# Kernel tuning notes

Hardware: AMD Instinct MI355X
Metric: run time of the kernel (lower is better)

## Reference

```python
import jax, jax.numpy as jnp
import numpy as np

HIDDEN = 50
INPUT = 4

def setup_inputs() -> dict:
    key = jax.random.key(0)
    ks = jax.random.split(key, 7)
    B, T = 4096, 512
    s_ih = 1.0 / np.sqrt(HIDDEN)
    return {
        "x": jax.random.normal(ks[0], (B, T, INPUT), dtype=jnp.float32),
        "W_ih": jax.random.uniform(ks[1], (4 * HIDDEN, INPUT), jnp.float32, -s_ih, s_ih),
        "W_hh": jax.random.uniform(ks[2], (4 * HIDDEN, HIDDEN), jnp.float32, -s_ih, s_ih),
        "b_ih": jax.random.uniform(ks[3], (4 * HIDDEN,), jnp.float32, -s_ih, s_ih),
        "b_hh": jax.random.uniform(ks[4], (4 * HIDDEN,), jnp.float32, -s_ih, s_ih),
        "W_fc": jax.random.uniform(ks[5], (1, HIDDEN), jnp.float32, -s_ih, s_ih),
        "b_fc": jax.random.uniform(ks[6], (1,), jnp.float32, -s_ih, s_ih),
    }

def reference(x, W_ih, W_hh, b_ih, b_hh, W_fc, b_fc):
    B = x.shape[0]
    b = b_ih + b_hh  # fold biases once
    # precompute input projection for all timesteps: [B,T,4H]
    x_proj = jnp.einsum('btd,gd->btg', x, W_ih) + b
    h0 = jnp.zeros((B, HIDDEN), x.dtype)
    c0 = jnp.zeros((B, HIDDEN), x.dtype)

    def step(carry, xp_t):
        h, c = carry
        gates = xp_t + h @ W_hh.T  # [B,4H]
        i, f, g, o = jnp.split(gates, 4, axis=-1)  # PyTorch gate order i,f,g,o
        i = jax.nn.sigmoid(i)
        f = jax.nn.sigmoid(f)
        g = jnp.tanh(g)
        o = jax.nn.sigmoid(o)
        c_new = f * c + i * g
        h_new = o * jnp.tanh(c_new)
        return (h_new, c_new), None

    (h_T, _), _ = jax.lax.scan(step, (h0, c0), jnp.swapaxes(x_proj, 0, 1))
    # fc applied to last timestep only (out[:, -1, :])
    return h_T @ W_fc.T + b_fc  # [B,1]
```

## Files before the change

### kernel.cpp

```cpp
#include <hip/hip_runtime.h>


#define HID  50
#define NROW 200
#define TT   512
#define NIN  4
#define BT   16
#define KD   72
#define XSTR 17
#define NW   8

typedef float f32x4 __attribute__((ext_vector_type(4)));
typedef short s16x8 __attribute__((ext_vector_type(8)));

__device__ __forceinline__ unsigned short f2bf(float f) {
    unsigned u = __builtin_bit_cast(unsigned, f);
    return (unsigned short)((u + 0x7FFF + ((u >> 16) & 1)) >> 16);
}
__device__ __forceinline__ float fast_sigmoid(float v) {
    float e = __builtin_amdgcn_exp2f(v * -1.442695040888963f);
    return __builtin_amdgcn_rcpf(1.0f + e);
}
__device__ __forceinline__ float fast_tanh(float v) {
    float e = __builtin_amdgcn_exp2f(v * -2.885390081777927f);
    return 2.0f * __builtin_amdgcn_rcpf(1.0f + e) - 1.0f;
}

__device__ __forceinline__ float wval(const float* W_hh, const float* W_ih,
                                      int rowp, int kp) {
    if (rowp >= NROW) return 0.0f;
    const int u = rowp >> 2, g = rowp & 3;
    if (kp < HID)              return W_hh[(g * HID + u) * HID + kp];
    if (kp >= 56 && kp < 60)   return W_ih[(g * HID + u) * NIN + (kp - 56)];
    return 0.0f;
}

__global__ __launch_bounds__(64 * NW, 2)
void lstm_mfma4(const float* __restrict__ x,
                const float* __restrict__ W_ih,
                const float* __restrict__ W_hh,
                const float* __restrict__ b_ih,
                const float* __restrict__ b_hh,
                const float* __restrict__ W_fc,
                const float* __restrict__ b_fc,
                float* __restrict__ out)
{
    __shared__ __align__(16) unsigned short buf[2][BT][KD];
    __shared__ uint2 xpl[TT * XSTR];
    __shared__ float red[BT];

    const int tid = threadIdx.x;
    const int w   = tid >> 6;
    const int l   = tid & 63;
    const int lr  = l & 15;
    const int lg  = l >> 4;
    const int b0  = blockIdx.x * BT;

    for (int i = tid; i < 2 * BT * KD; i += 64 * NW)
        ((unsigned short*)buf)[i] = 0;
    if (tid < BT) red[tid] = 0.0f;

    {
        const float4* xs = (const float4*)(x + (size_t)b0 * TT * NIN);
#pragma unroll
        for (int it = 0; it < (TT * BT) / (64 * NW); ++it) {
            const int e = tid + it * 64 * NW;
            const float4 v = xs[e];
            unsigned lo, hi;
            asm("v_cvt_pk_bf16_f32 %0, %1, %2" : "=v"(lo) : "v"(v.x), "v"(v.y));
            asm("v_cvt_pk_bf16_f32 %0, %1, %2" : "=v"(hi) : "v"(v.z), "v"(v.w));
            const int brel = e >> 9, t = e & (TT - 1);
            xpl[t * XSTR + brel] = make_uint2(lo, hi);
        }
    }

    const bool two = (w < 5);
    const int  T0  = two ? w : (w + 5);
    const int  T1  = w + 5;

    s16x8 af0[2], af1[2];
    f32x4 bias0, bias1 = {0.f, 0.f, 0.f, 0.f};
    float wfc0 = 0.0f, wfc1 = 0.0f;
    {
        const int rowp = 16 * T0 + lr;
#pragma unroll
        for (int kh = 0; kh < 2; ++kh) {
            s16x8 f;
#pragma unroll
            for (int j = 0; j < 8; ++j)
                f[j] = (short)f2bf(wval(W_hh, W_ih, rowp, 32 * kh + 8 * lg + j));
            af0[kh] = f;
        }
#pragma unroll
        for (int r = 0; r < 4; ++r) {
            const int rr = 16 * T0 + 4 * lg + r;
            bias0[r] = (rr < NROW) ? (b_ih[(rr & 3) * HID + (rr >> 2)] +
                                      b_hh[(rr & 3) * HID + (rr >> 2)]) : 0.0f;
        }
        const int u = 4 * T0 + lg;
        wfc0 = (u < HID) ? W_fc[u] : 0.0f;
    }
    if (two) {
        const int rowp = 16 * T1 + lr;
#pragma unroll
        for (int kh = 0; kh < 2; ++kh) {
            s16x8 f;
#pragma unroll
            for (int j = 0; j < 8; ++j)
                f[j] = (short)f2bf(wval(W_hh, W_ih, rowp, 32 * kh + 8 * lg + j));
            af1[kh] = f;
        }
#pragma unroll
        for (int r = 0; r < 4; ++r) {
            const int rr = 16 * T1 + 4 * lg + r;
            bias1[r] = (rr < NROW) ? (b_ih[(rr & 3) * HID + (rr >> 2)] +
                                      b_hh[(rr & 3) * HID + (rr >> 2)]) : 0.0f;
        }
        const int u = 4 * T1 + lg;
        wfc1 = (u < HID) ? W_fc[u] : 0.0f;
    }
    __syncthreads();

    float c0 = 0.f, h0 = 0.f, c1 = 0.f, h1 = 0.f;

    for (int t = 0; t < TT; ++t) {
        const int p = t & 1;

        const s16x8 bf0v = *(const s16x8*)&buf[p][lr][8 * lg];
        s16x8 bf1v;
        if (lg == 3) {
            const uint2 xv = xpl[t * XSTR + lr];
            const uint4 tmp = {xv.x, xv.y, 0u, 0u};
            bf1v = __builtin_bit_cast(s16x8, tmp);
        } else {
            bf1v = *(const s16x8*)&buf[p][lr][32 + 8 * lg];
        }

        f32x4 a0 = bias0;
        a0 = __builtin_amdgcn_mfma_f32_16x16x32_bf16(af0[0], bf0v, a0, 0, 0, 0);
        a0 = __builtin_amdgcn_mfma_f32_16x16x32_bf16(af0[1], bf1v, a0, 0, 0, 0);
        f32x4 a1;
        if (two) {
            a1 = bias1;
            a1 = __builtin_amdgcn_mfma_f32_16x16x32_bf16(af1[0], bf0v, a1, 0, 0, 0);
            a1 = __builtin_amdgcn_mfma_f32_16x16x32_bf16(af1[1], bf1v, a1, 0, 0, 0);
        }

        {
            const float gi = fast_sigmoid(a0[0]);
            const float gf = fast_sigmoid(a0[1]);
            const float gg = fast_tanh(a0[2]);
            const float go = fast_sigmoid(a0[3]);
            c0 = gf * c0 + gi * gg;
            h0 = go * fast_tanh(c0);
            buf[p ^ 1][lr][4 * T0 + lg] = f2bf(h0);
        }
        if (two) {
            const float gi = fast_sigmoid(a1[0]);
            const float gf = fast_sigmoid(a1[1]);
            const float gg = fast_tanh(a1[2]);
            const float go = fast_sigmoid(a1[3]);
            c1 = gf * c1 + gi * gg;
            h1 = go * fast_tanh(c1);
            buf[p ^ 1][lr][4 * T1 + lg] = f2bf(h1);
        }
        __syncthreads();
    }

    float partial = wfc0 * h0 + wfc1 * h1;
    partial += __shfl_down(partial, 32);
    partial += __shfl_down(partial, 16);
    if (l < 16) atomicAdd(&red[l], partial);
    __syncthreads();
    if (tid < BT) out[b0 + tid] = red[tid] + b_fc[0];
}

extern "C" void kernel_launch(void* const* d_in, const int* in_sizes, int n_in,
                              void* d_out, int out_size, void* d_ws, size_t ws_size,
                              hipStream_t stream) {
    const float* x    = (const float*)d_in[0];
    const float* W_ih = (const float*)d_in[1];
    const float* W_hh = (const float*)d_in[2];
    const float* b_ih = (const float*)d_in[3];
    const float* b_hh = (const float*)d_in[4];
    const float* W_fc = (const float*)d_in[5];
    const float* b_fc = (const float*)d_in[6];
    float* out        = (float*)d_out;

    const int B = in_sizes[0] / (TT * NIN);
    lstm_mfma4<<<B / BT, 64 * NW, 0, stream>>>(x, W_ih, W_hh, b_ih, b_hh, W_fc, b_fc, out);
}
```

Baseline: 326.1 us.

## Halve batch per block, split MFMA accumulation chains, stage x into buffer

```diff
diff --git a/kernel.cpp b/kernel.cpp
--- a/kernel.cpp
+++ b/kernel.cpp
@@ -5,9 +5,8 @@
 #define NROW 200
 #define TT   512
 #define NIN  4
-#define BT   16
+#define BTO  8
 #define KD   72
-#define XSTR 17
 #define NW   8
 
 typedef float f32x4 __attribute__((ext_vector_type(4)));
@@ -35,8 +34,8 @@
     return 0.0f;
 }
 
-__global__ __launch_bounds__(64 * NW, 2)
-void lstm_mfma4(const float* __restrict__ x,
+__global__ __launch_bounds__(64 * NW, 4)
+void lstm_mfma5(const float* __restrict__ x,
                 const float* __restrict__ W_ih,
                 const float* __restrict__ W_hh,
                 const float* __restrict__ b_ih,
@@ -45,32 +44,32 @@
                 const float* __restrict__ b_fc,
                 float* __restrict__ out)
 {
-    __shared__ __align__(16) unsigned short buf[2][BT][KD];
-    __shared__ uint2 xpl[TT * XSTR];
-    __shared__ float red[BT];
+    __shared__ __align__(16) unsigned short buf[2][16][KD];
+    __shared__ uint2 xpl[TT * BTO];
+    __shared__ float red[16];
 
     const int tid = threadIdx.x;
     const int w   = tid >> 6;
     const int l   = tid & 63;
     const int lr  = l & 15;
     const int lg  = l >> 4;
-    const int b0  = blockIdx.x * BT;
+    const int b0  = blockIdx.x * BTO;
 
-    for (int i = tid; i < 2 * BT * KD; i += 64 * NW)
+    for (int i = tid; i < 2 * 16 * KD; i += 64 * NW)
         ((unsigned short*)buf)[i] = 0;
-    if (tid < BT) red[tid] = 0.0f;
+    if (tid < 16) red[tid] = 0.0f;
 
     {
         const float4* xs = (const float4*)(x + (size_t)b0 * TT * NIN);
 #pragma unroll
-        for (int it = 0; it < (TT * BT) / (64 * NW); ++it) {
+        for (int it = 0; it < (TT * BTO) / (64 * NW); ++it) {
             const int e = tid + it * 64 * NW;
             const float4 v = xs[e];
             unsigned lo, hi;
             asm("v_cvt_pk_bf16_f32 %0, %1, %2" : "=v"(lo) : "v"(v.x), "v"(v.y));
             asm("v_cvt_pk_bf16_f32 %0, %1, %2" : "=v"(hi) : "v"(v.z), "v"(v.w));
             const int brel = e >> 9, t = e & (TT - 1);
-            xpl[t * XSTR + brel] = make_uint2(lo, hi);
+            xpl[t * BTO + brel] = make_uint2(lo, hi);
         }
     }
 
@@ -121,45 +120,46 @@
     }
     __syncthreads();
 
+    if (w == 7 && l < BTO)
+        *(uint2*)&buf[0][l][56] = xpl[l];
+    __syncthreads();
+
     float c0 = 0.f, h0 = 0.f, c1 = 0.f, h1 = 0.f;
+    const f32x4 zero4 = {0.f, 0.f, 0.f, 0.f};
 
     for (int t = 0; t < TT; ++t) {
         const int p = t & 1;
 
         const s16x8 bf0v = *(const s16x8*)&buf[p][lr][8 * lg];
-        s16x8 bf1v;
-        if (lg == 3) {
-            const uint2 xv = xpl[t * XSTR + lr];
-            const uint4 tmp = {xv.x, xv.y, 0u, 0u};
-            bf1v = __builtin_bit_cast(s16x8, tmp);
-        } else {
-            bf1v = *(const s16x8*)&buf[p][lr][32 + 8 * lg];
+        const s16x8 bf1v = *(const s16x8*)&buf[p][lr][32 + 8 * lg];
+
+        f32x4 a0 = __builtin_amdgcn_mfma_f32_16x16x32_bf16(af0[0], bf0v, bias0, 0, 0, 0);
+        f32x4 a0b = __builtin_amdgcn_mfma_f32_16x16x32_bf16(af0[1], bf1v, zero4, 0, 0, 0);
+        f32x4 a1, a1b;
+        if (two) {
+            a1  = __builtin_amdgcn_mfma_f32_16x16x32_bf16(af1[0], bf0v, bias1, 0, 0, 0);
+            a1b = __builtin_amdgcn_mfma_f32_16x16x32_bf16(af1[1], bf1v, zero4, 0, 0, 0);
         }
 
-        f32x4 a0 = bias0;
-        a0 = __builtin_amdgcn_mfma_f32_16x16x32_bf16(af0[0], bf0v, a0, 0, 0, 0);
-        a0 = __builtin_amdgcn_mfma_f32_16x16x32_bf16(af0[1], bf1v, a0, 0, 0, 0);
-        f32x4 a1;
-        if (two) {
-            a1 = bias1;
-            a1 = __builtin_amdgcn_mfma_f32_16x16x32_bf16(af1[0], bf0v, a1, 0, 0, 0);
-            a1 = __builtin_amdgcn_mfma_f32_16x16x32_bf16(af1[1], bf1v, a1, 0, 0, 0);
-        }
+        if (w == 7 && l < BTO && t + 1 < TT)
+            *(uint2*)&buf[p ^ 1][l][56] = xpl[(t + 1) * BTO + l];
 
         {
-            const float gi = fast_sigmoid(a0[0]);
-            const float gf = fast_sigmoid(a0[1]);
-            const float gg = fast_tanh(a0[2]);
-            const float go = fast_sigmoid(a0[3]);
+            const f32x4 a = a0 + a0b;
+            const float gi = fast_sigmoid(a[0]);
+            const float gf = fast_sigmoid(a[1]);
+            const float gg = fast_tanh(a[2]);
+            const float go = fast_sigmoid(a[3]);
             c0 = gf * c0 + gi * gg;
             h0 = go * fast_tanh(c0);
             buf[p ^ 1][lr][4 * T0 + lg] = f2bf(h0);
         }
         if (two) {
-            const float gi = fast_sigmoid(a1[0]);
-            const float gf = fast_sigmoid(a1[1]);
-            const float gg = fast_tanh(a1[2]);
-            const float go = fast_sigmoid(a1[3]);
+            const f32x4 a = a1 + a1b;
+            const float gi = fast_sigmoid(a[0]);
+            const float gf = fast_sigmoid(a[1]);
+            const float gg = fast_tanh(a[2]);
+            const float go = fast_sigmoid(a[3]);
             c1 = gf * c1 + gi * gg;
             h1 = go * fast_tanh(c1);
             buf[p ^ 1][lr][4 * T1 + lg] = f2bf(h1);
@@ -172,7 +172,7 @@
     partial += __shfl_down(partial, 16);
     if (l < 16) atomicAdd(&red[l], partial);
     __syncthreads();
-    if (tid < BT) out[b0 + tid] = red[tid] + b_fc[0];
+    if (tid < BTO) out[b0 + tid] = red[tid] + b_fc[0];
 }
 
 extern "C" void kernel_launch(void* const* d_in, const int* in_sizes, int n_in,
@@ -188,5 +188,5 @@
     float* out        = (float*)d_out;
 
     const int B = in_sizes[0] / (TT * NIN);
-    lstm_mfma4<<<B / BT, 64 * NW, 0, stream>>>(x, W_ih, W_hh, b_ih, b_hh, W_fc, b_fc, out);
+    lstm_mfma5<<<B / BTO, 64 * NW, 0, stream>>>(x, W_ih, W_hh, b_ih, b_hh, W_fc, b_fc, out);
 }
```

Result: slower. 443.8 us (+36.1%).

## Halve waves per block, give each wave three or four gate tiles

Applied to the files above, without the earlier changes.

```diff
diff --git a/kernel.cpp b/kernel.cpp
--- a/kernel.cpp
+++ b/kernel.cpp
@@ -8,7 +8,7 @@
 #define BT   16
 #define KD   72
 #define XSTR 17
-#define NW   8
+#define NW   4
 
 typedef float f32x4 __attribute__((ext_vector_type(4)));
 typedef short s16x8 __attribute__((ext_vector_type(8)));
@@ -35,8 +35,8 @@
     return 0.0f;
 }
 
-__global__ __launch_bounds__(64 * NW, 2)
-void lstm_mfma4(const float* __restrict__ x,
+__global__ __launch_bounds__(64 * NW, 1)
+void lstm_mfma6(const float* __restrict__ x,
                 const float* __restrict__ W_ih,
                 const float* __restrict__ W_hh,
                 const float* __restrict__ b_ih,
@@ -74,103 +74,88 @@
         }
     }
 
-    const bool two = (w < 5);
-    const int  T0  = two ? w : (w + 5);
-    const int  T1  = w + 5;
-
-    s16x8 af0[2], af1[2];
-    f32x4 bias0, bias1 = {0.f, 0.f, 0.f, 0.f};
-    float wfc0 = 0.0f, wfc1 = 0.0f;
-    {
-        const int rowp = 16 * T0 + lr;
+    s16x8 af[4][2];
+    f32x4 bias[4];
+    float wfc[4];
+#pragma unroll
+    for (int j = 0; j < 4; ++j) {
+        const int T = w + 4 * j;
+        const int rowp = 16 * T + lr;
 #pragma unroll
         for (int kh = 0; kh < 2; ++kh) {
             s16x8 f;
 #pragma unroll
-            for (int j = 0; j < 8; ++j)
-                f[j] = (short)f2bf(wval(W_hh, W_ih, rowp, 32 * kh + 8 * lg + j));
-            af0[kh] = f;
+            for (int jj = 0; jj < 8; ++jj)
+                f[jj] = (short)f2bf(wval(W_hh, W_ih, rowp, 32 * kh + 8 * lg + jj));
+            af[j][kh] = f;
         }
+        f32x4 bv;
 #pragma unroll
         for (int r = 0; r < 4; ++r) {
-            const int rr = 16 * T0 + 4 * lg + r;
-            bias0[r] = (rr < NROW) ? (b_ih[(rr & 3) * HID + (rr >> 2)] +
-                                      b_hh[(rr & 3) * HID + (rr >> 2)]) : 0.0f;
+            const int rr = 16 * T + 4 * lg + r;
+            bv[r] = (rr < NROW) ? (b_ih[(rr & 3) * HID + (rr >> 2)] +
+                                   b_hh[(rr & 3) * HID + (rr >> 2)]) : 0.0f;
         }
-        const int u = 4 * T0 + lg;
-        wfc0 = (u < HID) ? W_fc[u] : 0.0f;
-    }
-    if (two) {
-        const int rowp = 16 * T1 + lr;
-#pragma unroll
-        for (int kh = 0; kh < 2; ++kh) {
-            s16x8 f;
-#pragma unroll
-            for (int j = 0; j < 8; ++j)
-                f[j] = (short)f2bf(wval(W_hh, W_ih, rowp, 32 * kh + 8 * lg + j));
-            af1[kh] = f;
-        }
-#pragma unroll
-        for (int r = 0; r < 4; ++r) {
-            const int rr = 16 * T1 + 4 * lg + r;
-            bias1[r] = (rr < NROW) ? (b_ih[(rr & 3) * HID + (rr >> 2)] +
-                                      b_hh[(rr & 3) * HID + (rr >> 2)]) : 0.0f;
-        }
-        const int u = 4 * T1 + lg;
-        wfc1 = (u < HID) ? W_fc[u] : 0.0f;
+        bias[j] = bv;
+        const int u = 4 * T + lg;
+        wfc[j] = (u < HID) ? W_fc[u] : 0.0f;
     }
     __syncthreads();
 
-    float c0 = 0.f, h0 = 0.f, c1 = 0.f, h1 = 0.f;
+    if (w == 1 && l < BT)
+        *(uint2*)&buf[0][l][56] = xpl[l];
+    __syncthreads();
+
+    float c[4] = {0.f, 0.f, 0.f, 0.f};
+    float h[4] = {0.f, 0.f, 0.f, 0.f};
 
     for (int t = 0; t < TT; ++t) {
         const int p = t & 1;
 
         const s16x8 bf0v = *(const s16x8*)&buf[p][lr][8 * lg];
-        s16x8 bf1v;
-        if (lg == 3) {
-            const uint2 xv = xpl[t * XSTR + lr];
-            const uint4 tmp = {xv.x, xv.y, 0u, 0u};
-            bf1v = __builtin_bit_cast(s16x8, tmp);
-        } else {
-            bf1v = *(const s16x8*)&buf[p][lr][32 + 8 * lg];
+        const s16x8 bf1v = *(const s16x8*)&buf[p][lr][32 + 8 * lg];
+
+        f32x4 a[4];
+#pragma unroll
+        for (int j = 0; j < 3; ++j) {
+            f32x4 acc = __builtin_amdgcn_mfma_f32_16x16x32_bf16(af[j][0], bf0v, bias[j], 0, 0, 0);
+            a[j]      = __builtin_amdgcn_mfma_f32_16x16x32_bf16(af[j][1], bf1v, acc,    0, 0, 0);
+        }
+        if (w == 0) {
+            f32x4 acc = __builtin_amdgcn_mfma_f32_16x16x32_bf16(af[3][0], bf0v, bias[3], 0, 0, 0);
+            a[3]      = __builtin_amdgcn_mfma_f32_16x16x32_bf16(af[3][1], bf1v, acc,    0, 0, 0);
         }
 
-        f32x4 a0 = bias0;
-        a0 = __builtin_amdgcn_mfma_f32_16x16x32_bf16(af0[0], bf0v, a0, 0, 0, 0);
-        a0 = __builtin_amdgcn_mfma_f32_16x16x32_bf16(af0[1], bf1v, a0, 0, 0, 0);
-        f32x4 a1;
-        if (two) {
-            a1 = bias1;
-            a1 = __builtin_amdgcn_mfma_f32_16x16x32_bf16(af1[0], bf0v, a1, 0, 0, 0);
-            a1 = __builtin_amdgcn_mfma_f32_16x16x32_bf16(af1[1], bf1v, a1, 0, 0, 0);
+        if (w == 1 && l < BT && t + 1 < TT)
+            *(uint2*)&buf[p ^ 1][l][56] = xpl[(t + 1) * XSTR + l];
+
+#pragma unroll
+        for (int j = 0; j < 3; ++j) {
+            const float gi = fast_sigmoid(a[j][0]);
+            const float gf = fast_sigmoid(a[j][1]);
+            const float gg = fast_tanh(a[j][2]);
+            const float go = fast_sigmoid(a[j][3]);
+            c[j] = gf * c[j] + gi * gg;
+            h[j] = go * fast_tanh(c[j]);
+            buf[p ^ 1][lr][4 * (w + 4 * j) + lg] = f2bf(h[j]);
         }
-
-        {
-            const float gi = fast_sigmoid(a0[0]);
-            const float gf = fast_sigmoid(a0[1]);
-            const float gg = fast_tanh(a0[2]);
-            const float go = fast_sigmoid(a0[3]);
-            c0 = gf * c0 + gi * gg;
-            h0 = go * fast_tanh(c0);
-            buf[p ^ 1][lr][4 * T0 + lg] = f2bf(h0);
-        }
-        if (two) {
-            const float gi = fast_sigmoid(a1[0]);
-            const float gf = fast_sigmoid(a1[1]);
-            const float gg = fast_tanh(a1[2]);
-            const float go = fast_sigmoid(a1[3]);
-            c1 = gf * c1 + gi * gg;
-            h1 = go * fast_tanh(c1);
-            buf[p ^ 1][lr][4 * T1 + lg] = f2bf(h1);
+        if (w == 0) {
+            const float gi = fast_sigmoid(a[3][0]);
+            const float gf = fast_sigmoid(a[3][1]);
+            const float gg = fast_tanh(a[3][2]);
+            const float go = fast_sigmoid(a[3][3]);
+            c[3] = gf * c[3] + gi * gg;
+            h[3] = go * fast_tanh(c[3]);
+            buf[p ^ 1][lr][48 + lg] = f2bf(h[3]);
         }
         __syncthreads();
     }
 
-    float partial = wfc0 * h0 + wfc1 * h1;
+    float partial = wfc[0] * h[0] + wfc[1] * h[1] + wfc[2] * h[2];
+    if (w == 0) partial += wfc[3] * h[3];
     partial += __shfl_down(partial, 32);
     partial += __shfl_down(partial, 16);
-    if (l < 16) atomicAdd(&red[l], partial);
+    if (l < BT) atomicAdd(&red[l], partial);
     __syncthreads();
     if (tid < BT) out[b0 + tid] = red[tid] + b_fc[0];
 }
@@ -188,5 +173,5 @@
     float* out        = (float*)d_out;
 
     const int B = in_sizes[0] / (TT * NIN);
-    lstm_mfma4<<<B / BT, 64 * NW, 0, stream>>>(x, W_ih, W_hh, b_ih, b_hh, W_fc, b_fc, out);
+    lstm_mfma6<<<B / BT, 64 * NW, 0, stream>>>(x, W_ih, W_hh, b_ih, b_hh, W_fc, b_fc, out);
 }
```

New measurement: 335.9 us. 3.0% more time.
